# Kernel tuning notes

Hardware: AMD Instinct MI355X
Metric: run time of the kernel (lower is better)

## Reference

```python
import math
import jax, jax.numpy as jnp
import numpy as np

B, S, DM, H, KH = 2, 2048, 1024, 16, 4
HD = DM // H          # 64
N_REP = H // KH       # 4
ROPE_THETA = 10000.0


def setup_inputs() -> dict:
    key = jax.random.key(0)
    ks = jax.random.split(key, 5)
    x = jax.random.normal(ks[0], (B, S, DM), dtype=jnp.float32)
    wq = jax.random.normal(ks[1], (H * HD, DM), dtype=jnp.float32) * 0.02
    wk = jax.random.normal(ks[2], (KH * HD, DM), dtype=jnp.float32) * 0.02
    wv = jax.random.normal(ks[3], (KH * HD, DM), dtype=jnp.float32) * 0.02
    wo = jax.random.normal(ks[4], (DM, H * HD), dtype=jnp.float32) * 0.02
    # freqs_cis = exp(i * t * theta^(-2j/d)) represented as cos/sin, shape [S, HD//2]
    inv_freq = 1.0 / (ROPE_THETA ** (jnp.arange(0, HD, 2, dtype=jnp.float32) / HD))
    angles = jnp.arange(S, dtype=jnp.float32)[:, None] * inv_freq[None, :]
    return {
        'x': x, 'wq': wq, 'wk': wk, 'wv': wv, 'wo': wo,
        'freqs_cos': jnp.cos(angles), 'freqs_sin': jnp.sin(angles),
    }


def _rope(t, cos, sin):
    # t: [B, S, h, HD]; pairs (even, odd) rotated as complex mul
    tr = t.reshape(*t.shape[:-1], HD // 2, 2)
    xr, xi = tr[..., 0], tr[..., 1]
    c = cos[None, :, None, :]  # [1, S, 1, HD//2]
    s = sin[None, :, None, :]
    out = jnp.stack([xr * c - xi * s, xr * s + xi * c], axis=-1)
    return out.reshape(t.shape)


def reference(x, wq, wk, wv, wo, freqs_cos, freqs_sin):
    b, s, _ = x.shape
    xq = (x @ wq.T).reshape(b, s, H, HD)
    xk = (x @ wk.T).reshape(b, s, KH, HD)
    xv = (x @ wv.T).reshape(b, s, KH, HD)
    xq = _rope(xq, freqs_cos, freqs_sin)
    xk = _rope(xk, freqs_cos, freqs_sin)
    # [B, h, S, HD]
    xq = xq.transpose(0, 2, 1, 3)
    xk = xk.transpose(0, 2, 1, 3)
    xv = xv.transpose(0, 2, 1, 3)
    # GQA: repeat_interleave kv heads to match query heads
    xk = jnp.repeat(xk, N_REP, axis=1)
    xv = jnp.repeat(xv, N_REP, axis=1)
    scale = 1.0 / math.sqrt(HD)
    scores = jnp.einsum('bhqd,bhkd->bhqk', xq, xk) * scale
    causal = jnp.tril(jnp.ones((s, s), dtype=bool))
    scores = jnp.where(causal[None, None], scores, jnp.finfo(scores.dtype).min)
    attn = jax.nn.softmax(scores, axis=-1)
    out = jnp.einsum('bhqk,bhkd->bhqd', attn, xv)
    out = out.transpose(0, 2, 1, 3).reshape(b, s, H * HD)
    return out @ wo.T
```

## Files before the change

### kernel.cpp

```cpp
#include <hip/hip_runtime.h>
#include <hip/hip_bf16.h>
#include <type_traits>

#define B_ 2
#define S_ 2048
#define DM_ 1024
#define H_ 16
#define KH_ 4
#define HD_ 64
#define NREP_ 4
#define QKV_LD 1536
#define CLOG 0.1803368801111244f
#define FIXM 8.0f

typedef float f32x4 __attribute__((ext_vector_type(4)));
typedef float f32x16 __attribute__((ext_vector_type(16)));
typedef short s16x8 __attribute__((ext_vector_type(8)));
typedef unsigned int u32x2 __attribute__((ext_vector_type(2)));

static __device__ __forceinline__ float bf2f(unsigned short u) {
  union { unsigned int u; float f; } x; x.u = ((unsigned int)u) << 16; return x.f;
}
static __device__ __forceinline__ unsigned short f2bf(float f) {
  union { float f; unsigned int u; } x; x.f = f;
  unsigned int r = (x.u + 0x7fffu + ((x.u >> 16) & 1u)) >> 16;
  return (unsigned short)r;
}
static __device__ __forceinline__ unsigned int cvtpk_bf16(float lo, float hi) {
  unsigned int r;
  asm("v_cvt_pk_bf16_f32 %0, %1, %2" : "=v"(r) : "v"(lo), "v"(hi));
  return r;
}
static __device__ __forceinline__ float fexp2(float x) {
  float r;
  asm("v_exp_f32 %0, %1" : "=v"(r) : "v"(x));
  return r;
}

__device__ __forceinline__ void gload_lds16(const unsigned short* g, unsigned short* l) {
  __builtin_amdgcn_global_load_lds(
      (const __attribute__((address_space(1))) unsigned int*)g,
      (__attribute__((address_space(3))) unsigned int*)l, 16, 0, 0);
}

__global__ void cvt_all_k(const float* __restrict__ x,
                          const float* __restrict__ wq, const float* __restrict__ wk,
                          const float* __restrict__ wv, const float* __restrict__ wo,
                          unsigned short* __restrict__ xb,
                          unsigned short* __restrict__ wqkv, unsigned short* __restrict__ wob) {
  int i = (blockIdx.x * 256 + threadIdx.x) * 4;
  const float* src; unsigned short* dst; int off;
  if (i < 4194304)      { src = x;  dst = xb;              off = i; }
  else if (i < 5242880) { src = wq; dst = wqkv;            off = i - 4194304; }
  else if (i < 5505024) { src = wk; dst = wqkv + 1048576;  off = i - 5242880; }
  else if (i < 5767168) { src = wv; dst = wqkv + 1310720;  off = i - 5505024; }
  else                  { src = wo; dst = wob;             off = i - 5767168; }
  float4 v = *(const float4*)(src + off);
  ushort4 o;
  o.x = f2bf(v.x); o.y = f2bf(v.y); o.z = f2bf(v.z); o.w = f2bf(v.w);
  *(ushort4*)(dst + off) = o;
}

#define BM 128
#define BN 128
#define BK 32

template <typename OT>
__global__ __launch_bounds__(512) void gemm_bt(const unsigned short* __restrict__ A,
                                               const unsigned short* __restrict__ Bw,
                                               OT* __restrict__ C,
                                               int M, int N, int K) {
  __shared__ unsigned short lds_a[BM * BK];
  __shared__ unsigned short lds_b[BN * BK];
  const int tid = threadIdx.x;
  const int wave = tid >> 6, lane = tid & 63;
  const int lr = lane & 15, lg = lane >> 4;
  const int m0 = blockIdx.y * BM, n0 = blockIdx.x * BN;
  const int wr = wave >> 2, wc = wave & 3;

  f32x4 acc[4][2] = {};

  const int srow = tid >> 2, scol = (tid & 3) << 3;

  for (int k0 = 0; k0 < K; k0 += BK) {
    gload_lds16(A + (size_t)(m0 + srow) * K + k0 + scol, &lds_a[tid * 8]);
    gload_lds16(Bw + (size_t)(n0 + srow) * K + k0 + scol, &lds_b[tid * 8]);
    __syncthreads();
    s16x8 af[4], bfr[2];
    #pragma unroll
    for (int mi = 0; mi < 4; ++mi)
      af[mi] = *(const s16x8*)&lds_a[(wr * 64 + mi * 16 + lr) * BK + lg * 8];
    #pragma unroll
    for (int ni = 0; ni < 2; ++ni)
      bfr[ni] = *(const s16x8*)&lds_b[(wc * 32 + ni * 16 + lr) * BK + lg * 8];
    #pragma unroll
    for (int mi = 0; mi < 4; ++mi) {
      #pragma unroll
      for (int ni = 0; ni < 2; ++ni)
        acc[mi][ni] = __builtin_amdgcn_mfma_f32_16x16x32_bf16(af[mi], bfr[ni], acc[mi][ni], 0, 0, 0);
    }
    __syncthreads();
  }
  #pragma unroll
  for (int mi = 0; mi < 4; ++mi) {
    #pragma unroll
    for (int ni = 0; ni < 2; ++ni) {
      #pragma unroll
      for (int r = 0; r < 4; ++r) {
        int row = m0 + wr * 64 + mi * 16 + lg * 4 + r;
        int col = n0 + wc * 32 + ni * 16 + lr;
        if constexpr (std::is_same<OT, unsigned short>::value)
          C[(size_t)row * N + col] = f2bf(acc[mi][ni][r]);
        else
          C[(size_t)row * N + col] = acc[mi][ni][r];
      }
    }
  }
}

__global__ void kvpack_k(const unsigned short* __restrict__ qkv,
                         const float* __restrict__ fc, const float* __restrict__ fs,
                         unsigned short* __restrict__ kp, unsigned short* __restrict__ vp) {
  int idx = blockIdx.x * 256 + threadIdx.x;
  int lane = idx & 63;
  int f  = (idx >> 6) & 3;
  int t  = (idx >> 8) & 63;
  int p  = idx >> 14;
  int b = p >> 2, kh = p & 3;
  int ql = lane & 31, hi = lane >> 5;
  {
    int s = t * 32 + ql;
    int d0 = f * 16 + hi * 8;
    const unsigned short* src = qkv + (size_t)(b * S_ + s) * QKV_LD + 1024 + kh * HD_ + d0;
    s16x8 v = *(const s16x8*)src;
    int i0 = d0 >> 1;
    float4 c4 = *(const float4*)(fc + s * 32 + i0);
    float4 s4 = *(const float4*)(fs + s * 32 + i0);
    float cc[4] = {c4.x, c4.y, c4.z, c4.w};
    float ss[4] = {s4.x, s4.y, s4.z, s4.w};
    union { s16x8 v; unsigned int w[4]; } o;
    #pragma unroll
    for (int e = 0; e < 4; ++e) {
      float xr = bf2f((unsigned short)v[2 * e]);
      float xi = bf2f((unsigned short)v[2 * e + 1]);
      o.w[e] = cvtpk_bf16(xr * cc[e] - xi * ss[e], xr * ss[e] + xi * cc[e]);
    }
    *(s16x8*)(kp + (size_t)idx * 8) = o.v;
  }
  {
    int d = (f >> 1) * 32 + ql;
    int kv0 = t * 32 + (f & 1) * 16 + hi * 8;
    const unsigned short* src = qkv + (size_t)(b * S_ + kv0) * QKV_LD + 1280 + kh * HD_ + d;
    s16x8 o;
    #pragma unroll
    for (int e = 0; e < 8; ++e) o[e] = (short)src[(size_t)e * QKV_LD];
    *(s16x8*)(vp + (size_t)idx * 8) = o;
  }
}

__global__ __launch_bounds__(256, 3) void attn_fwd10(const unsigned short* __restrict__ qkv,
                                                     const unsigned short* __restrict__ kp,
                                                     const unsigned short* __restrict__ vp,
                                                     const float* __restrict__ fc,
                                                     const float* __restrict__ fs,
                                                     unsigned short* __restrict__ ob) {
  __shared__ float mbuf[2][64][34];
  const int tid = threadIdx.x;
  const int wave = tid >> 6, lane = tid & 63;
  const int ql = lane & 31;
  const int hi = lane >> 5;
  const int bi = blockIdx.x;
  const int xcd = bi & 7;
  const int b = xcd >> 2, kh = xcd & 3;
  const int j = bi >> 3;
  const int h = kh * NREP_ + (j & 3);
  const int bt = j >> 2;

  int c, t0, t1;
  int sW1buf = -1, sM1buf = -1;
  bool sW2 = false, sM2 = false, doOut;
  if (bt < 32) {
    c = 63 - bt;
    int T = c + 1;
    t0 = (wave * T) >> 2; t1 = ((wave + 1) * T) >> 2;
    sW1buf = (wave == 1) ? 0 : (wave == 3) ? 1 : -1;
    sM1buf = (wave == 0) ? 0 : (wave == 2) ? 1 : -1;
    sW2 = (wave == 2); sM2 = (wave == 0);
    doOut = (wave == 0);
  } else if (bt < 40) {
    int bb2 = bt - 32;
    c = (wave < 2) ? (16 + bb2) : (31 - bb2);
    int T = c + 1, Th = T >> 1;
    if ((wave & 1) == 0) { t0 = 0;  t1 = Th; } else { t0 = Th; t1 = T; }
    sW1buf = (wave == 1) ? 0 : (wave == 3) ? 1 : -1;
    sM1buf = (wave == 0) ? 0 : (wave == 2) ? 1 : -1;
    doOut = (wave == 0) || (wave == 2);
  } else {
    c = (bt - 40) * 4 + wave;
    t0 = 0; t1 = c + 1;
    doOut = true;
  }
  const int q = c * 32 + ql;

  const unsigned short* qrow = qkv + (size_t)(b * S_ + q) * QKV_LD + h * HD_;
  s16x8 qf[4];
  #pragma unroll
  for (int ks = 0; ks < 4; ++ks) {
    s16x8 v = *(const s16x8*)(qrow + ks * 16 + hi * 8);
    int i0 = ks * 8 + hi * 4;
    float4 c4 = *(const float4*)(fc + q * 32 + i0);
    float4 s4 = *(const float4*)(fs + q * 32 + i0);
    float cc[4] = {c4.x, c4.y, c4.z, c4.w};
    float ss[4] = {s4.x, s4.y, s4.z, s4.w};
    union { s16x8 v; unsigned int w[4]; } o;
    #pragma unroll
    for (int e = 0; e < 4; ++e) {
      float xr = bf2f((unsigned short)v[2 * e]);
      float xi = bf2f((unsigned short)v[2 * e + 1]);
      o.w[e] = cvtpk_bf16(xr * cc[e] - xi * ss[e], xr * ss[e] + xi * cc[e]);
    }
    qf[ks] = o.v;
  }

  const unsigned short* kpt = kp + ((size_t)(b * KH_ + kh) << 17) + lane * 8;
  const unsigned short* vpt = vp + ((size_t)(b * KH_ + kh) << 17) + lane * 8;

  f32x16 oT0 = {};
  f32x16 oT1 = {};
  float l = 0.f;

  s16x8 ka[4], va[4], kb2[4], vb2[4];

#define LOADKV(T, KK, VV) do { \
    const unsigned short* kp_ = kpt + ((size_t)(T) << 11); \
    KK[0] = *(const s16x8*)(kp_);        KK[1] = *(const s16x8*)(kp_ + 512); \
    KK[2] = *(const s16x8*)(kp_ + 1024); KK[3] = *(const s16x8*)(kp_ + 1536); \
    const unsigned short* vp_ = vpt + ((size_t)(T) << 11); \
    VV[0] = *(const s16x8*)(vp_);        VV[1] = *(const s16x8*)(vp_ + 512); \
    VV[2] = *(const s16x8*)(vp_ + 1024); VV[3] = *(const s16x8*)(vp_ + 1536); \
  } while (0)

  auto body = [&](s16x8 (&KK)[4], s16x8 (&VV)[4], bool diag) __attribute__((always_inline)) {
    f32x16 st = {};
    __builtin_amdgcn_s_setprio(1);
    st = __builtin_amdgcn_mfma_f32_32x32x16_bf16(KK[0], qf[0], st, 0, 0, 0);
    st = __builtin_amdgcn_mfma_f32_32x32x16_bf16(KK[1], qf[1], st, 0, 0, 0);
    st = __builtin_amdgcn_mfma_f32_32x32x16_bf16(KK[2], qf[2], st, 0, 0, 0);
    st = __builtin_amdgcn_mfma_f32_32x32x16_bf16(KK[3], qf[3], st, 0, 0, 0);
    __builtin_amdgcn_s_setprio(0);
    if (diag) {
      #pragma unroll
      for (int r = 0; r < 16; ++r)
        if (((r & 3) + 8 * (r >> 2) + 4 * hi) > ql) st[r] = -1e30f;
    }
    float pr[16];
    #pragma unroll
    for (int r = 0; r < 16; ++r) pr[r] = fexp2(fmaf(st[r], CLOG, -FIXM));
    float s0 = (pr[0] + pr[1]) + (pr[2] + pr[3]);
    float s1 = (pr[4] + pr[5]) + (pr[6] + pr[7]);
    float s2 = (pr[8] + pr[9]) + (pr[10] + pr[11]);
    float s3 = (pr[12] + pr[13]) + (pr[14] + pr[15]);
    l += (s0 + s1) + (s2 + s3);
    #pragma unroll
    for (int ksv = 0; ksv < 2; ++ksv) {
      unsigned int a01 = cvtpk_bf16(pr[ksv * 8 + 0], pr[ksv * 8 + 1]);
      unsigned int a23 = cvtpk_bf16(pr[ksv * 8 + 2], pr[ksv * 8 + 3]);
      unsigned int b45 = cvtpk_bf16(pr[ksv * 8 + 4], pr[ksv * 8 + 5]);
      unsigned int b67 = cvtpk_bf16(pr[ksv * 8 + 6], pr[ksv * 8 + 7]);
      asm volatile("v_permlane32_swap_b32 %0, %1" : "+v"(a01), "+v"(b45));
      asm volatile("v_permlane32_swap_b32 %0, %1" : "+v"(a23), "+v"(b67));
      union { s16x8 v; unsigned int w[4]; } pb;
      pb.w[0] = a01; pb.w[1] = a23; pb.w[2] = b45; pb.w[3] = b67;
      __builtin_amdgcn_s_setprio(1);
      oT0 = __builtin_amdgcn_mfma_f32_32x32x16_bf16(VV[ksv], pb.v, oT0, 0, 0, 0);
      oT1 = __builtin_amdgcn_mfma_f32_32x32x16_bf16(VV[2 + ksv], pb.v, oT1, 0, 0, 0);
      __builtin_amdgcn_s_setprio(0);
    }
  };

  LOADKV(t0, ka, va);
  int t = t0;
  while (t + 1 < t1) {
    LOADKV(t + 1, kb2, vb2);
    body(ka, va, t == c);
    ++t;
    if (t + 1 < t1) LOADKV(t + 1, ka, va);
    body(kb2, vb2, t == c);
    ++t;
  }
  if (t < t1) body(ka, va, t == c);
#undef LOADKV

#define WRITEP(BUF) do { float* mp_ = &mbuf[BUF][lane][0]; \
    _Pragma("unroll") for (int r = 0; r < 16; ++r) { mp_[r] = oT0[r]; mp_[16 + r] = oT1[r]; } \
    mp_[32] = l; } while (0)
#define MERGEP(BUF) do { float* mp_ = &mbuf[BUF][lane][0]; \
    l += mp_[32]; \
    _Pragma("unroll") for (int r = 0; r < 16; ++r) { \
      oT0[r] += mp_[r]; \
      oT1[r] += mp_[16 + r]; } } while (0)

  __syncthreads();
  if (sW1buf >= 0) WRITEP(sW1buf);
  __syncthreads();
  if (sM1buf >= 0) MERGEP(sM1buf);
  __syncthreads();
  if (sW2) WRITEP(0);
  __syncthreads();
  if (sM2) MERGEP(0);
#undef WRITEP
#undef MERGEP

  if (doOut) {
    float l_tot = l + __shfl_xor(l, 32);
    float invl = 1.0f / l_tot;
    unsigned short* orow = ob + (size_t)(b * S_ + q) * DM_ + h * HD_;
    #pragma unroll
    for (int dblk = 0; dblk < 2; ++dblk) {
      #pragma unroll
      for (int g = 0; g < 4; ++g) {
        float e0 = (dblk ? oT1[4 * g + 0] : oT0[4 * g + 0]) * invl;
        float e1 = (dblk ? oT1[4 * g + 1] : oT0[4 * g + 1]) * invl;
        float e2 = (dblk ? oT1[4 * g + 2] : oT0[4 * g + 2]) * invl;
        float e3 = (dblk ? oT1[4 * g + 3] : oT0[4 * g + 3]) * invl;
        u32x2 w;
        w.x = cvtpk_bf16(e0, e1);
        w.y = cvtpk_bf16(e2, e3);
        *(u32x2*)(orow + dblk * 32 + g * 8 + 4 * hi) = w;
      }
    }
  }
}

extern "C" void kernel_launch(void* const* d_in, const int* in_sizes, int n_in,
                              void* d_out, int out_size, void* d_ws, size_t ws_size,
                              hipStream_t stream) {
  const float* x  = (const float*)d_in[0];
  const float* wq = (const float*)d_in[1];
  const float* wk = (const float*)d_in[2];
  const float* wv = (const float*)d_in[3];
  const float* wo = (const float*)d_in[4];
  const float* fc = (const float*)d_in[5];
  const float* fs = (const float*)d_in[6];
  float* out = (float*)d_out;

  const size_t nX    = (size_t)B_ * S_ * DM_;
  const size_t nWQKV = (size_t)QKV_LD * DM_;
  const size_t nWO   = (size_t)DM_ * DM_;
  const size_t nQKV  = (size_t)B_ * S_ * QKV_LD;
  const size_t nKV   = (size_t)B_ * S_ * KH_ * HD_;

  unsigned short* xb    = (unsigned short*)d_ws;
  unsigned short* wqkv  = xb + nX;
  unsigned short* wob   = wqkv + nWQKV;
  unsigned short* qkv   = wob + nWO;
  unsigned short* kpk   = qkv + nQKV;
  unsigned short* vpk   = kpk + nKV;
  unsigned short* a_buf = vpk + nKV;

  const int M = B_ * S_;

  cvt_all_k<<<6656, 256, 0, stream>>>(x, wq, wk, wv, wo, xb, wqkv, wob);

  gemm_bt<unsigned short><<<dim3(QKV_LD / BN, M / BM), 512, 0, stream>>>(
      xb, wqkv, qkv, M, QKV_LD, DM_);

  kvpack_k<<<512, 256, 0, stream>>>(qkv, fc, fs, kpk, vpk);

  attn_fwd10<<<1408, 256, 0, stream>>>(qkv, kpk, vpk, fc, fs, a_buf);

  gemm_bt<float><<<dim3(DM_ / BN, M / BM), 512, 0, stream>>>(
      a_buf, wob, out, M, DM_, DM_);
}
```

Measured before the change: 98.92 us.

## Single-buffer K/V prefetch in attention loop and raise occupancy to four blocks

The attention inner loop previously double-buffered both K and V tiles in registers. Now a single set is kept: the next K tile is loaded right after the QK MFMAs and the next V tile after the PV MFMAs. Exp and packing are also split per half-tile, which lowers peak register use. Together these allow launch bounds of 4 blocks per CU instead of 3. The trade is less load latency hiding within each wave in exchange for more waves resident per CU.

```diff
diff --git a/kernel.cpp b/kernel.cpp
--- a/kernel.cpp
+++ b/kernel.cpp
@@ -158,7 +158,7 @@
   }
 }
 
-__global__ __launch_bounds__(256, 3) void attn_fwd10(const unsigned short* __restrict__ qkv,
+__global__ __launch_bounds__(256, 4) void attn_fwd12(const unsigned short* __restrict__ qkv,
                                                      const unsigned short* __restrict__ kp,
                                                      const unsigned short* __restrict__ vp,
                                                      const float* __restrict__ fc,
@@ -229,67 +229,61 @@
   f32x16 oT1 = {};
   float l = 0.f;
 
-  s16x8 ka[4], va[4], kb2[4], vb2[4];
-
-#define LOADKV(T, KK, VV) do { \
+  s16x8 ka[4], va[4];
+
+#define LOADK(T) do { \
     const unsigned short* kp_ = kpt + ((size_t)(T) << 11); \
-    KK[0] = *(const s16x8*)(kp_);        KK[1] = *(const s16x8*)(kp_ + 512); \
-    KK[2] = *(const s16x8*)(kp_ + 1024); KK[3] = *(const s16x8*)(kp_ + 1536); \
+    ka[0] = *(const s16x8*)(kp_);        ka[1] = *(const s16x8*)(kp_ + 512); \
+    ka[2] = *(const s16x8*)(kp_ + 1024); ka[3] = *(const s16x8*)(kp_ + 1536); \
+  } while (0)
+#define LOADV(T) do { \
     const unsigned short* vp_ = vpt + ((size_t)(T) << 11); \
-    VV[0] = *(const s16x8*)(vp_);        VV[1] = *(const s16x8*)(vp_ + 512); \
-    VV[2] = *(const s16x8*)(vp_ + 1024); VV[3] = *(const s16x8*)(vp_ + 1536); \
+    va[0] = *(const s16x8*)(vp_);        va[1] = *(const s16x8*)(vp_ + 512); \
+    va[2] = *(const s16x8*)(vp_ + 1024); va[3] = *(const s16x8*)(vp_ + 1536); \
   } while (0)
 
-  auto body = [&](s16x8 (&KK)[4], s16x8 (&VV)[4], bool diag) __attribute__((always_inline)) {
+  LOADK(t0);
+  LOADV(t0);
+  for (int t = t0; t < t1; ++t) {
+    const bool diag = (t == c);
+    const bool more = (t + 1 < t1);
     f32x16 st = {};
     __builtin_amdgcn_s_setprio(1);
-    st = __builtin_amdgcn_mfma_f32_32x32x16_bf16(KK[0], qf[0], st, 0, 0, 0);
-    st = __builtin_amdgcn_mfma_f32_32x32x16_bf16(KK[1], qf[1], st, 0, 0, 0);
-    st = __builtin_amdgcn_mfma_f32_32x32x16_bf16(KK[2], qf[2], st, 0, 0, 0);
-    st = __builtin_amdgcn_mfma_f32_32x32x16_bf16(KK[3], qf[3], st, 0, 0, 0);
+    st = __builtin_amdgcn_mfma_f32_32x32x16_bf16(ka[0], qf[0], st, 0, 0, 0);
+    st = __builtin_amdgcn_mfma_f32_32x32x16_bf16(ka[1], qf[1], st, 0, 0, 0);
+    st = __builtin_amdgcn_mfma_f32_32x32x16_bf16(ka[2], qf[2], st, 0, 0, 0);
+    st = __builtin_amdgcn_mfma_f32_32x32x16_bf16(ka[3], qf[3], st, 0, 0, 0);
     __builtin_amdgcn_s_setprio(0);
+    if (more) LOADK(t + 1);
     if (diag) {
       #pragma unroll
       for (int r = 0; r < 16; ++r)
         if (((r & 3) + 8 * (r >> 2) + 4 * hi) > ql) st[r] = -1e30f;
     }
-    float pr[16];
-    #pragma unroll
-    for (int r = 0; r < 16; ++r) pr[r] = fexp2(fmaf(st[r], CLOG, -FIXM));
-    float s0 = (pr[0] + pr[1]) + (pr[2] + pr[3]);
-    float s1 = (pr[4] + pr[5]) + (pr[6] + pr[7]);
-    float s2 = (pr[8] + pr[9]) + (pr[10] + pr[11]);
-    float s3 = (pr[12] + pr[13]) + (pr[14] + pr[15]);
-    l += (s0 + s1) + (s2 + s3);
     #pragma unroll
     for (int ksv = 0; ksv < 2; ++ksv) {
-      unsigned int a01 = cvtpk_bf16(pr[ksv * 8 + 0], pr[ksv * 8 + 1]);
-      unsigned int a23 = cvtpk_bf16(pr[ksv * 8 + 2], pr[ksv * 8 + 3]);
-      unsigned int b45 = cvtpk_bf16(pr[ksv * 8 + 4], pr[ksv * 8 + 5]);
-      unsigned int b67 = cvtpk_bf16(pr[ksv * 8 + 6], pr[ksv * 8 + 7]);
+      float pr[8];
+      #pragma unroll
+      for (int e = 0; e < 8; ++e)
+        pr[e] = fexp2(fmaf(st[ksv * 8 + e], CLOG, -FIXM));
+      l += ((pr[0] + pr[1]) + (pr[2] + pr[3])) + ((pr[4] + pr[5]) + (pr[6] + pr[7]));
+      unsigned int a01 = cvtpk_bf16(pr[0], pr[1]);
+      unsigned int a23 = cvtpk_bf16(pr[2], pr[3]);
+      unsigned int b45 = cvtpk_bf16(pr[4], pr[5]);
+      unsigned int b67 = cvtpk_bf16(pr[6], pr[7]);
       asm volatile("v_permlane32_swap_b32 %0, %1" : "+v"(a01), "+v"(b45));
       asm volatile("v_permlane32_swap_b32 %0, %1" : "+v"(a23), "+v"(b67));
       union { s16x8 v; unsigned int w[4]; } pb;
       pb.w[0] = a01; pb.w[1] = a23; pb.w[2] = b45; pb.w[3] = b67;
       __builtin_amdgcn_s_setprio(1);
-      oT0 = __builtin_amdgcn_mfma_f32_32x32x16_bf16(VV[ksv], pb.v, oT0, 0, 0, 0);
-      oT1 = __builtin_amdgcn_mfma_f32_32x32x16_bf16(VV[2 + ksv], pb.v, oT1, 0, 0, 0);
+      oT0 = __builtin_amdgcn_mfma_f32_32x32x16_bf16(va[ksv], pb.v, oT0, 0, 0, 0);
+      oT1 = __builtin_amdgcn_mfma_f32_32x32x16_bf16(va[2 + ksv], pb.v, oT1, 0, 0, 0);
       __builtin_amdgcn_s_setprio(0);
     }
-  };
-
-  LOADKV(t0, ka, va);
-  int t = t0;
-  while (t + 1 < t1) {
-    LOADKV(t + 1, kb2, vb2);
-    body(ka, va, t == c);
-    ++t;
-    if (t + 1 < t1) LOADKV(t + 1, ka, va);
-    body(kb2, vb2, t == c);
-    ++t;
-  }
-  if (t < t1) body(ka, va, t == c);
-#undef LOADKV
+    if (more) LOADV(t + 1);
+  }
+#undef LOADK
+#undef LOADV
 
 #define WRITEP(BUF) do { float* mp_ = &mbuf[BUF][lane][0]; \
     _Pragma("unroll") for (int r = 0; r < 16; ++r) { mp_[r] = oT0[r]; mp_[16 + r] = oT1[r]; } \
@@ -367,7 +361,7 @@
 
   kvpack_k<<<512, 256, 0, stream>>>(qkv, fc, fs, kpk, vpk);
 
-  attn_fwd10<<<1408, 256, 0, stream>>>(qkv, kpk, vpk, fc, fs, a_buf);
+  attn_fwd12<<<1408, 256, 0, stream>>>(qkv, kpk, vpk, fc, fs, a_buf);
 
   gemm_bt<float><<<dim3(DM_ / BN, M / BM), 512, 0, stream>>>(
       a_buf, wob, out, M, DM_, DM_);
```

After: 100.1 us. No clear change (+1.1%).
